# Performance work log

Hardware: AMD Instinct MI355X
Metric: run time of the kernel (lower is better)

## Reference

```python
import jax, jax.numpy as jnp
import numpy as np


def setup_inputs() -> dict:
    key = jax.random.key(0)
    k1, k2, k3, k4 = jax.random.split(key, 4)
    B, T, C, H = 8, 2048, 768, 64
    x = jax.random.normal(k1, (B, T, C), dtype=jnp.float32)
    # nn.Linear(n_embd, head_size, bias=False): weight [H, C]; stored here as [C, H] for x @ W
    Wk = jax.random.normal(k2, (C, H), dtype=jnp.float32) * (C ** -0.5)
    Wq = jax.random.normal(k3, (C, H), dtype=jnp.float32) * (C ** -0.5)
    Wv = jax.random.normal(k4, (C, H), dtype=jnp.float32) * (C ** -0.5)
    return {"x": x, "Wk": Wk, "Wq": Wq, "Wv": Wv}


def reference(x, Wk, Wq, Wv):
    # x: [B, T, C]
    C = x.shape[-1]
    k = jnp.einsum("btc,ch->bth", x, Wk)  # [B, T, H]
    q = jnp.einsum("btc,ch->bth", x, Wq)  # [B, T, H]
    v = jnp.einsum("btc,ch->bth", x, Wv)  # [B, T, H]
    # NOTE: source scales by C**-0.5 where C = n_embd (input channels), not head_size
    wei = jnp.einsum("bth,bsh->bts", q, k) * (C ** -0.5)  # [B, T, T]
    wei = jax.nn.softmax(wei, axis=-1)
    # dropout p=0.0 (eval): identity
    out = jnp.einsum("bts,bsh->bth", wei, v)  # [B, T, H]
    return out
```

## Files before the change

kernel.cpp:

```cpp
#include <hip/hip_runtime.h>


typedef __attribute__((ext_vector_type(4))) float f32x4;
typedef __attribute__((ext_vector_type(8))) unsigned short u16x8;
typedef __attribute__((ext_vector_type(8))) __bf16 bf16x8;
typedef __attribute__((ext_vector_type(8))) _Float16 f16x8;

#define LDR 72
#define LDT 40
#define KSCALE (0.03608439182435161f * 1.4426950408889634f)
#define PBIAS 4.0f

__device__ __forceinline__ unsigned short f2bf(float f) {
  unsigned int u = __float_as_uint(f);
  u += 0x7FFFu + ((u >> 16) & 1u);
  return (unsigned short)(u >> 16);
}
__device__ __forceinline__ unsigned short hi16(float f) {
  return (unsigned short)(__float_as_uint(f) >> 16);
}
__device__ __forceinline__ f32x4 mfma_bf16(u16x8 a, u16x8 b, f32x4 c) {
  return __builtin_amdgcn_mfma_f32_16x16x32_bf16(
      __builtin_bit_cast(bf16x8, a), __builtin_bit_cast(bf16x8, b), c, 0, 0, 0);
}
__device__ __forceinline__ void cp32B(unsigned short* dst, const unsigned short* src) {
  *(u16x8*)dst = *(const u16x8*)src;
  *(u16x8*)(dst + 8) = *(const u16x8*)(src + 8);
}

__global__ __launch_bounds__(256) void wconv_k(const float* __restrict__ Wk,
                                               const float* __restrict__ Wq,
                                               const float* __restrict__ Wv,
                                               unsigned short* __restrict__ wt) {
  __shared__ unsigned short tr[64 * LDR];
  const int w = blockIdx.x / 12;
  const int kt = blockIdx.x - w * 12;
  const float* W = (w == 0) ? Wk : ((w == 1) ? Wq : Wv);
  const int tid = threadIdx.x;
  const int kr = tid >> 2;
  const int n0 = (tid & 3) * 16;
  const f32x4* src = (const f32x4*)(W + (size_t)(kt * 64 + kr) * 64 + n0);
  f32x4 a0 = src[0], a1 = src[1], a2 = src[2], a3 = src[3];
#pragma unroll
  for (int j = 0; j < 4; ++j) {
    tr[(n0 + j) * LDR + kr] = f2bf(a0[j]);
    tr[(n0 + 4 + j) * LDR + kr] = f2bf(a1[j]);
    tr[(n0 + 8 + j) * LDR + kr] = f2bf(a2[j]);
    tr[(n0 + 12 + j) * LDR + kr] = f2bf(a3[j]);
  }
  __syncthreads();
  const int n = tid >> 2, kc = (tid & 3) * 16;
  cp32B(&wt[(size_t)(w * 64 + n) * 768 + kt * 64 + kc], &tr[n * LDR + kc]);
}

__global__ __launch_bounds__(256) void proj_k(const float* __restrict__ x,
                                              const unsigned short* __restrict__ wt,
                                              unsigned short* __restrict__ kg,
                                              unsigned short* __restrict__ qg,
                                              unsigned short* __restrict__ vt) {
  __shared__ unsigned short x_s[32 * LDR];
  __shared__ unsigned short w_s[192 * LDR];
  __shared__ unsigned short vt_s[64 * LDT];
  const int tid = threadIdx.x;
  const int wv = tid >> 6, lane = tid & 63, c = lane & 15, quad = lane >> 4;
  const int m0 = blockIdx.x * 32;
  const int rowg = wv & 1;
  const int nfb = (wv >> 1) * 6;
  const int srow = tid >> 3;
  const int sc8 = (tid & 7) * 8;

  f32x4 acc[6];
#pragma unroll
  for (int i = 0; i < 6; ++i) acc[i] = f32x4{0.f, 0.f, 0.f, 0.f};

  f32x4 xf0, xf1;
  u16x8 wf[6];
  {
    const f32x4* s = (const f32x4*)(x + (size_t)(m0 + srow) * 768 + sc8);
    xf0 = s[0]; xf1 = s[1];
  }
#pragma unroll
  for (int i = 0; i < 6; ++i)
    wf[i] = *(const u16x8*)&wt[(size_t)(srow + 32 * i) * 768 + sc8];

  for (int kc = 0; kc < 768; kc += 64) {
    {
      u16x8 u;
#pragma unroll
      for (int j = 0; j < 4; ++j) { u[j] = f2bf(xf0[j]); u[4 + j] = f2bf(xf1[j]); }
      *(u16x8*)&x_s[srow * LDR + sc8] = u;
    }
#pragma unroll
    for (int i = 0; i < 6; ++i)
      *(u16x8*)&w_s[(srow + 32 * i) * LDR + sc8] = wf[i];
    __syncthreads();
    if (kc + 64 < 768) {
      const f32x4* s = (const f32x4*)(x + (size_t)(m0 + srow) * 768 + kc + 64 + sc8);
      xf0 = s[0]; xf1 = s[1];
#pragma unroll
      for (int i = 0; i < 6; ++i)
        wf[i] = *(const u16x8*)&wt[(size_t)(srow + 32 * i) * 768 + kc + 64 + sc8];
    }
#pragma unroll
    for (int k32 = 0; k32 < 2; ++k32) {
      u16x8 a = *(const u16x8*)&x_s[(rowg * 16 + c) * LDR + k32 * 32 + quad * 8];
#pragma unroll
      for (int j = 0; j < 6; ++j) {
        u16x8 b = *(const u16x8*)&w_s[((nfb + j) * 16 + c) * LDR + k32 * 32 + quad * 8];
        acc[j] = mfma_bf16(a, b, acc[j]);
      }
    }
    __syncthreads();
  }
  const int r0 = rowg * 16 + quad * 4;
#pragma unroll
  for (int j = 0; j < 6; ++j) {
    const int nf = nfb + j;
    if (nf < 4) {
#pragma unroll
      for (int r = 0; r < 4; ++r)
        kg[(size_t)(m0 + r0 + r) * 64 + nf * 16 + c] = f2bf(acc[j][r]);
    } else if (nf < 8) {
#pragma unroll
      for (int r = 0; r < 4; ++r)
        qg[(size_t)(m0 + r0 + r) * 64 + (nf - 4) * 16 + c] = f2bf(acc[j][r] * KSCALE);
    } else {
#pragma unroll
      for (int r = 0; r < 4; ++r)
        vt_s[((nf - 8) * 16 + c) * LDT + r0 + r] = f2bf(acc[j][r]);
    }
  }
  __syncthreads();
  {
    const int h = tid >> 2, c8 = (tid & 3) * 8;
    const int b = m0 >> 11, tb = m0 & 2047;
    *(u16x8*)(vt + (size_t)b * 131072 + (size_t)h * 2048 + tb + c8) =
        *(const u16x8*)&vt_s[h * LDT + c8];
  }
}

__global__ __launch_bounds__(256, 4) void attn_k(const unsigned short* __restrict__ qg,
                                                 const unsigned short* __restrict__ kg,
                                                 const unsigned short* __restrict__ vt,
                                                 _Float16* __restrict__ part,
                                                 float* __restrict__ lsum) {
  __shared__ unsigned short k_s[64 * LDR];
  __shared__ unsigned short v_s[64 * LDR];
  __shared__ unsigned short p_s[64 * LDR];
  const int tid = threadIdx.x;
  const int wv = tid >> 6, lane = tid & 63, c = lane & 15, quad = lane >> 4;
  const int bq = blockIdx.x;
  const int qt = blockIdx.y;
  const int sc = blockIdx.z;
  const int tq0 = qt * 64;
  const int srow = tid >> 2, sch = (tid & 3) * 16;
  const int s_beg = sc << 8, s_end = s_beg + 256;

  const unsigned short* kbase = kg + (size_t)bq * 131072;
  const unsigned short* vbase = vt + (size_t)bq * 131072;

  u16x8 aq[2];
#pragma unroll
  for (int k32 = 0; k32 < 2; ++k32)
    aq[k32] = *(const u16x8*)(qg + (size_t)(bq * 2048 + tq0 + wv * 16 + c) * 64 +
                              k32 * 32 + quad * 8);

  u16x8 kb0 = *(const u16x8*)(kbase + (size_t)(s_beg + srow) * 64 + sch);
  u16x8 kb1 = *(const u16x8*)(kbase + (size_t)(s_beg + srow) * 64 + sch + 8);
  u16x8 vb0 = *(const u16x8*)(vbase + (size_t)srow * 2048 + s_beg + sch);
  u16x8 vb1 = *(const u16x8*)(vbase + (size_t)srow * 2048 + s_beg + sch + 8);

  u16x8 ones;
#pragma unroll
  for (int j = 0; j < 8; ++j) ones[j] = 0x3F80;

  f32x4 o_acc[4], l_acc;
#pragma unroll
  for (int hf = 0; hf < 4; ++hf) o_acc[hf] = f32x4{0.f, 0.f, 0.f, 0.f};
  l_acc = f32x4{0.f, 0.f, 0.f, 0.f};

  for (int s0 = s_beg; s0 < s_end; s0 += 64) {
    *(u16x8*)&k_s[srow * LDR + sch] = kb0;
    *(u16x8*)&k_s[srow * LDR + sch + 8] = kb1;
    *(u16x8*)&v_s[srow * LDR + sch] = vb0;
    *(u16x8*)&v_s[srow * LDR + sch + 8] = vb1;
    __syncthreads();
    if (s0 + 64 < s_end) {
      kb0 = *(const u16x8*)(kbase + (size_t)(s0 + 64 + srow) * 64 + sch);
      kb1 = *(const u16x8*)(kbase + (size_t)(s0 + 64 + srow) * 64 + sch + 8);
      vb0 = *(const u16x8*)(vbase + (size_t)srow * 2048 + s0 + 64 + sch);
      vb1 = *(const u16x8*)(vbase + (size_t)srow * 2048 + s0 + 64 + sch + 8);
    }
    f32x4 sacc[4];
#pragma unroll
    for (int nf = 0; nf < 4; ++nf) sacc[nf] = f32x4{0.f, 0.f, 0.f, 0.f};
#pragma unroll
    for (int k32 = 0; k32 < 2; ++k32) {
#pragma unroll
      for (int nf = 0; nf < 4; ++nf) {
        u16x8 b = *(const u16x8*)&k_s[(nf * 16 + c) * LDR + k32 * 32 + quad * 8];
        sacc[nf] = mfma_bf16(aq[k32], b, sacc[nf]);
      }
    }
    const int prow = wv * 16 + quad * 4;
#pragma unroll
    for (int nf = 0; nf < 4; ++nf)
#pragma unroll
      for (int r = 0; r < 4; ++r)
        p_s[(prow + r) * LDR + ((nf ^ quad) * 16) + c] =
            hi16(__builtin_amdgcn_exp2f(sacc[nf][r] - PBIAS));
    asm volatile("s_waitcnt lgkmcnt(0)" ::: "memory");
#pragma unroll
    for (int k32 = 0; k32 < 2; ++k32) {
      const int chunkP = (2 * k32 + (quad >> 1)) ^ (c >> 2);
      u16x8 ap = *(const u16x8*)&p_s[(wv * 16 + c) * LDR + chunkP * 16 + (quad & 1) * 8];
#pragma unroll
      for (int hf = 0; hf < 4; ++hf) {
        u16x8 bv = *(const u16x8*)&v_s[(hf * 16 + c) * LDR + k32 * 32 + quad * 8];
        o_acc[hf] = mfma_bf16(ap, bv, o_acc[hf]);
      }
      l_acc = mfma_bf16(ap, ones, l_acc);
    }
    __syncthreads();
  }
  const int pbase = (bq * 32 + qt) * 8 + sc;
  _Float16* po = part + (size_t)pbase * 4096;
#pragma unroll
  for (int hf = 0; hf < 4; ++hf)
#pragma unroll
    for (int r = 0; r < 4; ++r)
      po[(wv * 16 + quad * 4 + r) * 64 + hf * 16 + c] = (_Float16)o_acc[hf][r];
  if (c == 0) {
#pragma unroll
    for (int r = 0; r < 4; ++r)
      lsum[pbase * 64 + wv * 16 + quad * 4 + r] = l_acc[r];
  }
}

__global__ __launch_bounds__(256) void comb_k(const _Float16* __restrict__ part,
                                              const float* __restrict__ lsum,
                                              float* __restrict__ out) {
  const int bq = blockIdx.x, qh = blockIdx.y;
  const int qt = qh >> 1;
  const int row = (qh & 1) * 32 + (threadIdx.x >> 3);
  const int h0 = (threadIdx.x & 7) * 8;
  const int base = (bq * 32 + qt) * 8;
  float acc[8];
#pragma unroll
  for (int j = 0; j < 8; ++j) acc[j] = 0.f;
  float l = 0.f;
#pragma unroll
  for (int c8 = 0; c8 < 8; ++c8) {
    l += lsum[(base + c8) * 64 + row];
    f16x8 p = *(const f16x8*)(part + (size_t)(base + c8) * 4096 + row * 64 + h0);
#pragma unroll
    for (int j = 0; j < 8; ++j) acc[j] += (float)p[j];
  }
  const float inv = 1.0f / l;
  float* op = out + (size_t)(bq * 2048 + qt * 64 + row) * 64 + h0;
#pragma unroll
  for (int j = 0; j < 8; ++j) op[j] = acc[j] * inv;
}

extern "C" void kernel_launch(void* const* d_in, const int* in_sizes, int n_in,
                              void* d_out, int out_size, void* d_ws, size_t ws_size,
                              hipStream_t stream) {
  const float* x = (const float*)d_in[0];
  const float* Wk = (const float*)d_in[1];
  const float* Wq = (const float*)d_in[2];
  const float* Wv = (const float*)d_in[3];
  char* ws = (char*)d_ws;
  unsigned short* kg = (unsigned short*)(ws);
  unsigned short* qg = (unsigned short*)(ws + (size_t)(2 << 20));
  unsigned short* vt = (unsigned short*)(ws + (size_t)(4 << 20));
  unsigned short* wt = (unsigned short*)(ws + (size_t)(6 << 20));
  _Float16* part = (_Float16*)(ws + (size_t)(7 << 20));
  float* lsum = (float*)(ws + (size_t)(23 << 20));
  float* out = (float*)d_out;

  hipLaunchKernelGGL(wconv_k, dim3(36), dim3(256), 0, stream, Wk, Wq, Wv, wt);
  hipLaunchKernelGGL(proj_k, dim3(512), dim3(256), 0, stream, x, wt, kg, qg, vt);
  hipLaunchKernelGGL(attn_k, dim3(8, 32, 8), dim3(256), 0, stream, qg, kg, vt, part, lsum);
  hipLaunchKernelGGL(comb_k, dim3(8, 64), dim3(256), 0, stream, part, lsum, out);
}
```

Baseline: 122.3 us.

## Drop shared K/V staging and process 32 query rows per wave

The attention kernel no longer stages K and V through shared memory with block-wide barriers. Each wave loads its K and V fragments straight from global memory into registers and handles 32 query rows, so each block covers 128 queries and the grid halves. The score MFMA swaps operands so P can be written to shared memory as packed 4-element vectors. Per-wave global traffic rises and register pressure grows (launch bounds lowered to 3 blocks), while barriers and LDS round trips are removed. The combine kernel is reindexed for the 128-row partial layout.

Result: slower. 137.8 us (+12.6%).

```diff
diff --git a/kernel.cpp b/kernel.cpp
--- a/kernel.cpp
+++ b/kernel.cpp
@@ -2,6 +2,7 @@
 
 
 typedef __attribute__((ext_vector_type(4))) float f32x4;
+typedef __attribute__((ext_vector_type(4))) unsigned short u16x4;
 typedef __attribute__((ext_vector_type(8))) unsigned short u16x8;
 typedef __attribute__((ext_vector_type(8))) __bf16 bf16x8;
 typedef __attribute__((ext_vector_type(8))) _Float16 f16x8;
@@ -139,125 +140,135 @@
   }
 }
 
-__global__ __launch_bounds__(256, 4) void attn_k(const unsigned short* __restrict__ qg,
+__global__ __launch_bounds__(256, 3) void attn_k(const unsigned short* __restrict__ qg,
                                                  const unsigned short* __restrict__ kg,
                                                  const unsigned short* __restrict__ vt,
                                                  _Float16* __restrict__ part,
                                                  float* __restrict__ lsum) {
-  __shared__ unsigned short k_s[64 * LDR];
-  __shared__ unsigned short v_s[64 * LDR];
-  __shared__ unsigned short p_s[64 * LDR];
+  __shared__ unsigned short p_s[128 * LDR];
   const int tid = threadIdx.x;
   const int wv = tid >> 6, lane = tid & 63, c = lane & 15, quad = lane >> 4;
   const int bq = blockIdx.x;
   const int qt = blockIdx.y;
   const int sc = blockIdx.z;
-  const int tq0 = qt * 64;
-  const int srow = tid >> 2, sch = (tid & 3) * 16;
-  const int s_beg = sc << 8, s_end = s_beg + 256;
+  const int q0 = qt * 128 + wv * 32;
+  const int s_beg = sc << 8;
 
   const unsigned short* kbase = kg + (size_t)bq * 131072;
   const unsigned short* vbase = vt + (size_t)bq * 131072;
 
-  u16x8 aq[2];
-#pragma unroll
-  for (int k32 = 0; k32 < 2; ++k32)
-    aq[k32] = *(const u16x8*)(qg + (size_t)(bq * 2048 + tq0 + wv * 16 + c) * 64 +
-                              k32 * 32 + quad * 8);
-
-  u16x8 kb0 = *(const u16x8*)(kbase + (size_t)(s_beg + srow) * 64 + sch);
-  u16x8 kb1 = *(const u16x8*)(kbase + (size_t)(s_beg + srow) * 64 + sch + 8);
-  u16x8 vb0 = *(const u16x8*)(vbase + (size_t)srow * 2048 + s_beg + sch);
-  u16x8 vb1 = *(const u16x8*)(vbase + (size_t)srow * 2048 + s_beg + sch + 8);
+  u16x8 aq[2][2];
+#pragma unroll
+  for (int m = 0; m < 2; ++m)
+#pragma unroll
+    for (int k32 = 0; k32 < 2; ++k32)
+      aq[m][k32] = *(const u16x8*)(qg + (size_t)(bq * 2048 + q0 + m * 16 + c) * 64 +
+                                   k32 * 32 + quad * 8);
 
   u16x8 ones;
 #pragma unroll
   for (int j = 0; j < 8; ++j) ones[j] = 0x3F80;
 
-  f32x4 o_acc[4], l_acc;
-#pragma unroll
-  for (int hf = 0; hf < 4; ++hf) o_acc[hf] = f32x4{0.f, 0.f, 0.f, 0.f};
-  l_acc = f32x4{0.f, 0.f, 0.f, 0.f};
-
-  for (int s0 = s_beg; s0 < s_end; s0 += 64) {
-    *(u16x8*)&k_s[srow * LDR + sch] = kb0;
-    *(u16x8*)&k_s[srow * LDR + sch + 8] = kb1;
-    *(u16x8*)&v_s[srow * LDR + sch] = vb0;
-    *(u16x8*)&v_s[srow * LDR + sch + 8] = vb1;
-    __syncthreads();
-    if (s0 + 64 < s_end) {
-      kb0 = *(const u16x8*)(kbase + (size_t)(s0 + 64 + srow) * 64 + sch);
-      kb1 = *(const u16x8*)(kbase + (size_t)(s0 + 64 + srow) * 64 + sch + 8);
-      vb0 = *(const u16x8*)(vbase + (size_t)srow * 2048 + s0 + 64 + sch);
-      vb1 = *(const u16x8*)(vbase + (size_t)srow * 2048 + s0 + 64 + sch + 8);
-    }
-    f32x4 sacc[4];
-#pragma unroll
-    for (int nf = 0; nf < 4; ++nf) sacc[nf] = f32x4{0.f, 0.f, 0.f, 0.f};
-#pragma unroll
-    for (int k32 = 0; k32 < 2; ++k32) {
+  f32x4 o_acc[2][4];
+  f32x4 l_acc[2];
+#pragma unroll
+  for (int m = 0; m < 2; ++m) {
+#pragma unroll
+    for (int hf = 0; hf < 4; ++hf) o_acc[m][hf] = f32x4{0.f, 0.f, 0.f, 0.f};
+    l_acc[m] = f32x4{0.f, 0.f, 0.f, 0.f};
+  }
+  const int prow0 = wv * 32;
+
+  for (int s0 = s_beg; s0 < s_beg + 256; s0 += 64) {
+    u16x8 kf[2][4];
+#pragma unroll
+    for (int k32 = 0; k32 < 2; ++k32)
+#pragma unroll
+      for (int nf = 0; nf < 4; ++nf)
+        kf[k32][nf] = *(const u16x8*)(kbase + (size_t)(s0 + nf * 16 + c) * 64 +
+                                      k32 * 32 + quad * 8);
+    f32x4 st[2][4];
+#pragma unroll
+    for (int m = 0; m < 2; ++m)
+#pragma unroll
+      for (int nf = 0; nf < 4; ++nf) st[m][nf] = f32x4{0.f, 0.f, 0.f, 0.f};
+#pragma unroll
+    for (int k32 = 0; k32 < 2; ++k32)
+#pragma unroll
+      for (int m = 0; m < 2; ++m)
+#pragma unroll
+        for (int nf = 0; nf < 4; ++nf)
+          st[m][nf] = mfma_bf16(kf[k32][nf], aq[m][k32], st[m][nf]);
+#pragma unroll
+    for (int m = 0; m < 2; ++m)
 #pragma unroll
       for (int nf = 0; nf < 4; ++nf) {
-        u16x8 b = *(const u16x8*)&k_s[(nf * 16 + c) * LDR + k32 * 32 + quad * 8];
-        sacc[nf] = mfma_bf16(aq[k32], b, sacc[nf]);
+        u16x4 w;
+#pragma unroll
+        for (int r = 0; r < 4; ++r)
+          w[r] = hi16(__builtin_amdgcn_exp2f(st[m][nf][r] - PBIAS));
+        *(u16x4*)&p_s[(prow0 + m * 16 + c) * LDR + nf * 16 + quad * 4] = w;
       }
-    }
-    const int prow = wv * 16 + quad * 4;
-#pragma unroll
-    for (int nf = 0; nf < 4; ++nf)
-#pragma unroll
-      for (int r = 0; r < 4; ++r)
-        p_s[(prow + r) * LDR + ((nf ^ quad) * 16) + c] =
-            hi16(__builtin_amdgcn_exp2f(sacc[nf][r] - PBIAS));
+    u16x8 vf[2][4];
+#pragma unroll
+    for (int s32 = 0; s32 < 2; ++s32)
+#pragma unroll
+      for (int hf = 0; hf < 4; ++hf)
+        vf[s32][hf] = *(const u16x8*)(vbase + (size_t)(hf * 16 + c) * 2048 + s0 +
+                                      s32 * 32 + quad * 8);
     asm volatile("s_waitcnt lgkmcnt(0)" ::: "memory");
 #pragma unroll
-    for (int k32 = 0; k32 < 2; ++k32) {
-      const int chunkP = (2 * k32 + (quad >> 1)) ^ (c >> 2);
-      u16x8 ap = *(const u16x8*)&p_s[(wv * 16 + c) * LDR + chunkP * 16 + (quad & 1) * 8];
-#pragma unroll
-      for (int hf = 0; hf < 4; ++hf) {
-        u16x8 bv = *(const u16x8*)&v_s[(hf * 16 + c) * LDR + k32 * 32 + quad * 8];
-        o_acc[hf] = mfma_bf16(ap, bv, o_acc[hf]);
+    for (int m = 0; m < 2; ++m)
+#pragma unroll
+      for (int s32 = 0; s32 < 2; ++s32) {
+        u16x8 ap = *(const u16x8*)&p_s[(prow0 + m * 16 + c) * LDR + s32 * 32 + quad * 8];
+#pragma unroll
+        for (int hf = 0; hf < 4; ++hf)
+          o_acc[m][hf] = mfma_bf16(ap, vf[s32][hf], o_acc[m][hf]);
+        l_acc[m] = mfma_bf16(ap, ones, l_acc[m]);
       }
-      l_acc = mfma_bf16(ap, ones, l_acc);
-    }
-    __syncthreads();
-  }
-  const int pbase = (bq * 32 + qt) * 8 + sc;
-  _Float16* po = part + (size_t)pbase * 4096;
-#pragma unroll
-  for (int hf = 0; hf < 4; ++hf)
-#pragma unroll
-    for (int r = 0; r < 4; ++r)
-      po[(wv * 16 + quad * 4 + r) * 64 + hf * 16 + c] = (_Float16)o_acc[hf][r];
+  }
+  const int pbase = (bq * 16 + qt) * 8 + sc;
+  _Float16* po = part + (size_t)pbase * 8192;
+#pragma unroll
+  for (int m = 0; m < 2; ++m)
+#pragma unroll
+    for (int hf = 0; hf < 4; ++hf)
+#pragma unroll
+      for (int r = 0; r < 4; ++r)
+        po[(wv * 32 + m * 16 + quad * 4 + r) * 64 + hf * 16 + c] =
+            (_Float16)o_acc[m][hf][r];
   if (c == 0) {
 #pragma unroll
-    for (int r = 0; r < 4; ++r)
-      lsum[pbase * 64 + wv * 16 + quad * 4 + r] = l_acc[r];
+    for (int m = 0; m < 2; ++m)
+#pragma unroll
+      for (int r = 0; r < 4; ++r)
+        lsum[pbase * 128 + wv * 32 + m * 16 + quad * 4 + r] = l_acc[m][r];
   }
 }
 
 __global__ __launch_bounds__(256) void comb_k(const _Float16* __restrict__ part,
                                               const float* __restrict__ lsum,
                                               float* __restrict__ out) {
-  const int bq = blockIdx.x, qh = blockIdx.y;
-  const int qt = qh >> 1;
-  const int row = (qh & 1) * 32 + (threadIdx.x >> 3);
+  const int bq = blockIdx.x, y = blockIdx.y;
+  const int qglob = y * 32 + (threadIdx.x >> 3);
+  const int tile = qglob >> 7;
+  const int row = qglob & 127;
   const int h0 = (threadIdx.x & 7) * 8;
-  const int base = (bq * 32 + qt) * 8;
+  const int base = (bq * 16 + tile) * 8;
   float acc[8];
 #pragma unroll
   for (int j = 0; j < 8; ++j) acc[j] = 0.f;
   float l = 0.f;
 #pragma unroll
   for (int c8 = 0; c8 < 8; ++c8) {
-    l += lsum[(base + c8) * 64 + row];
-    f16x8 p = *(const f16x8*)(part + (size_t)(base + c8) * 4096 + row * 64 + h0);
+    l += lsum[(base + c8) * 128 + row];
+    f16x8 p = *(const f16x8*)(part + (size_t)(base + c8) * 8192 + row * 64 + h0);
 #pragma unroll
     for (int j = 0; j < 8; ++j) acc[j] += (float)p[j];
   }
   const float inv = 1.0f / l;
-  float* op = out + (size_t)(bq * 2048 + qt * 64 + row) * 64 + h0;
+  float* op = out + (size_t)(bq * 2048 + qglob) * 64 + h0;
 #pragma unroll
   for (int j = 0; j < 8; ++j) op[j] = acc[j] * inv;
 }
@@ -280,6 +291,6 @@
 
   hipLaunchKernelGGL(wconv_k, dim3(36), dim3(256), 0, stream, Wk, Wq, Wv, wt);
   hipLaunchKernelGGL(proj_k, dim3(512), dim3(256), 0, stream, x, wt, kg, qg, vt);
-  hipLaunchKernelGGL(attn_k, dim3(8, 32, 8), dim3(256), 0, stream, qg, kg, vt, part, lsum);
+  hipLaunchKernelGGL(attn_k, dim3(8, 16, 8), dim3(256), 0, stream, qg, kg, vt, part, lsum);
   hipLaunchKernelGGL(comb_k, dim3(8, 64), dim3(256), 0, stream, part, lsum, out);
 }
```
